# Kernel optimization log

Hardware: AMD Instinct MI355X
Metric: run time of the kernel (lower is better)

## Reference

```python
import jax, jax.numpy as jnp
import numpy as np

B, N, DIM = 2, 1024, 256
DEPTH, HEADS, DIM_HEAD = 4, 4, 64
INNER = HEADS * DIM_HEAD
SCALE = DIM_HEAD ** -0.5
STEP, LAMBD, EPS = 0.1, 0.1, 1e-5


def cx(re, im):
    return jax.lax.complex(re, im)


def setup_inputs() -> dict:
    key = jax.random.key(0)
    ks = jax.random.split(key, 8)
    s = np.float32(1.0 / np.sqrt(DIM))
    f32 = jnp.float32
    return {
        "x_re": jax.random.normal(ks[0], (B, N, DIM), f32),
        "x_im": jax.random.normal(ks[1], (B, N, DIM), f32),
        "ln1_w_re": jnp.ones((DEPTH, DIM), f32),
        "ln1_w_im": jnp.zeros((DEPTH, DIM), f32),
        "ln1_b_re": jnp.zeros((DEPTH, DIM), f32),
        "ln1_b_im": jnp.zeros((DEPTH, DIM), f32),
        "qkv_re": jax.random.normal(ks[2], (DEPTH, INNER, DIM), f32) * s,
        "qkv_im": jax.random.normal(ks[3], (DEPTH, INNER, DIM), f32) * s,
        "out_w_re": jax.random.normal(ks[4], (DEPTH, DIM, INNER), f32) * s,
        "out_w_im": jax.random.normal(ks[5], (DEPTH, DIM, INNER), f32) * s,
        "out_b_re": jnp.zeros((DEPTH, DIM), f32),
        "out_b_im": jnp.zeros((DEPTH, DIM), f32),
        "ln2_w_re": jnp.ones((DEPTH, DIM), f32),
        "ln2_w_im": jnp.zeros((DEPTH, DIM), f32),
        "ln2_b_re": jnp.zeros((DEPTH, DIM), f32),
        "ln2_b_im": jnp.zeros((DEPTH, DIM), f32),
        "ff_re": jax.random.normal(ks[6], (DEPTH, DIM, DIM), f32) * s,
        "ff_im": jax.random.normal(ks[7], (DEPTH, DIM, DIM), f32) * s,
    }


def complex_layernorm(x, w, b):
    # per-component mean/var on real and imag (torch unbiased=False), complex sqrt
    mean = cx(jnp.mean(x.real, -1, keepdims=True), jnp.mean(x.imag, -1, keepdims=True))
    var = cx(jnp.var(x.real, -1, keepdims=True), jnp.var(x.imag, -1, keepdims=True))
    xn = (x - mean) / jnp.sqrt(var + EPS)
    return w * xn + b


def attention(x, Wqkv, Wout, bout):
    # torch Linear: y = x @ W^T ; shared qkv projection w
    w = jnp.einsum('bnd,ed->bne', x, Wqkv)              # [B,N,INNER]
    w = w.reshape(B, N, HEADS, DIM_HEAD).transpose(0, 2, 1, 3)  # [B,H,N,Dh]
    dots = jnp.einsum('bhnd,bhmd->bhnm', w, w.conj()) * SCALE   # complex scores
    mag = jnp.abs(dots)
    a = jax.nn.softmax(mag, axis=-1)                    # softmax on magnitudes
    ph = jnp.angle(dots)                                # polar reconstruction
    attn = cx(a * jnp.cos(ph), a * jnp.sin(ph))
    out = jnp.einsum('bhnm,bhmd->bhnd', attn, w)
    out = out.transpose(0, 2, 1, 3).reshape(B, N, INNER)
    return jnp.einsum('bne,de->bnd', out, Wout) + bout


def feedforward(x, W):
    # FeedForward type1: x1 = x W^T ; CReLU(x + step*x1 - step*lambd)
    x1 = jnp.einsum('bnd,ed->bne', x, W)
    z = x + STEP * x1 - STEP * LAMBD
    return cx(jax.nn.relu(z.real), jax.nn.relu(z.imag))


def reference(x_re, x_im, ln1_w_re, ln1_w_im, ln1_b_re, ln1_b_im,
              qkv_re, qkv_im, out_w_re, out_w_im, out_b_re, out_b_im,
              ln2_w_re, ln2_w_im, ln2_b_re, ln2_b_im, ff_re, ff_im):
    x = cx(x_re, x_im)
    for l in range(DEPTH):
        xn = complex_layernorm(x, cx(ln1_w_re[l], ln1_w_im[l]), cx(ln1_b_re[l], ln1_b_im[l]))
        grad_x = attention(xn, cx(qkv_re[l], qkv_im[l]), cx(out_w_re[l], out_w_im[l]),
                           cx(out_b_re[l], out_b_im[l])) + x
        xn2 = complex_layernorm(grad_x, cx(ln2_w_re[l], ln2_w_im[l]), cx(ln2_b_re[l], ln2_b_im[l]))
        x = feedforward(xn2, cx(ff_re[l], ff_im[l]))
    return x
```

## Files before the change

kernel.cpp:

```cpp
#include <hip/hip_runtime.h>
#include <math.h>

#define B_ 2
#define N_ 1024
#define DIM_ 256
#define DEPTH_ 4
#define HEADS_ 4
#define DHEAD_ 64
#define INNER_ 256
#define SCALE_ 0.125f
#define STEP_ 0.1f
#define LAMBD_ 0.1f
#define EPS_ 1e-5f

typedef __attribute__((ext_vector_type(8))) short short8;
typedef __attribute__((ext_vector_type(4))) float f32x4;

__device__ __forceinline__ unsigned short bf16_rne(float x) {
    unsigned u = __float_as_uint(x);
    unsigned r = (u + 0x7FFFu + ((u >> 16) & 1u)) >> 16;
    return (unsigned short)r;
}
__device__ __forceinline__ float bf16_tof(unsigned short h) {
    return __uint_as_float(((unsigned)h) << 16);
}
__device__ __forceinline__ void split2(float x, unsigned short& hi, unsigned short& lo) {
    hi = bf16_rne(x);
    lo = bf16_rne(x - bf16_tof(hi));
}
__device__ __forceinline__ f32x4 mfma16(short8 a, short8 b, f32x4 c) {
    return __builtin_amdgcn_mfma_f32_16x16x32_bf16(a, b, c, 0, 0, 0);
}
__device__ __forceinline__ short8 neg8(short8 v) {
    union { short8 s; unsigned u[4]; } a; a.s = v;
    a.u[0] ^= 0x80008000u; a.u[1] ^= 0x80008000u;
    a.u[2] ^= 0x80008000u; a.u[3] ^= 0x80008000u;
    return a.s;
}

__global__ __launch_bounds__(64)
void ln_kernel(const float* __restrict__ xr, const float* __restrict__ xi,
               const float* __restrict__ wr, const float* __restrict__ wi,
               const float* __restrict__ br, const float* __restrict__ bi,
               float* __restrict__ outr, float* __restrict__ outi,
               unsigned short* __restrict__ planes, int S) {
    int row = blockIdx.x;
    int lane = threadIdx.x;
    int base = row * DIM_ + lane * 4;

    float4 xr4 = *(const float4*)(xr + base);
    float4 xi4 = *(const float4*)(xi + base);
    float ar[4] = {xr4.x, xr4.y, xr4.z, xr4.w};
    float ai[4] = {xi4.x, xi4.y, xi4.z, xi4.w};

    float sr = ar[0] + ar[1] + ar[2] + ar[3];
    float si = ai[0] + ai[1] + ai[2] + ai[3];
#pragma unroll
    for (int o = 1; o < 64; o <<= 1) {
        sr += __shfl_xor(sr, o, 64);
        si += __shfl_xor(si, o, 64);
    }
    float mre = sr * (1.f / DIM_), mim = si * (1.f / DIM_);

    float drv[4], div[4];
    float vr = 0.f, vi = 0.f;
#pragma unroll
    for (int j = 0; j < 4; j++) {
        drv[j] = ar[j] - mre;
        div[j] = ai[j] - mim;
        vr += drv[j] * drv[j];
        vi += div[j] * div[j];
    }
#pragma unroll
    for (int o = 1; o < 64; o <<= 1) {
        vr += __shfl_xor(vr, o, 64);
        vi += __shfl_xor(vi, o, 64);
    }
    float c = vr * (1.f / DIM_) + EPS_;
    float d = vi * (1.f / DIM_);
    float r = sqrtf(c * c + d * d);
    float sre = sqrtf(0.5f * (r + c));
    float sim = sqrtf(fmaxf(0.5f * (r - c), 0.f));
    float inv = 1.f / r;

    int wc = lane * 4;
    float4 wr4 = *(const float4*)(wr + wc);
    float4 wi4 = *(const float4*)(wi + wc);
    float4 br4 = *(const float4*)(br + wc);
    float4 bi4 = *(const float4*)(bi + wc);
    float wrv[4] = {wr4.x, wr4.y, wr4.z, wr4.w};
    float wiv[4] = {wi4.x, wi4.y, wi4.z, wi4.w};
    float brv[4] = {br4.x, br4.y, br4.z, br4.w};
    float biv[4] = {bi4.x, bi4.y, bi4.z, bi4.w};

    float orr[4], oii[4];
    unsigned short rh[4], rl[4], ih[4], il[4];
#pragma unroll
    for (int j = 0; j < 4; j++) {
        float nr = (drv[j] * sre + div[j] * sim) * inv;
        float ni = (div[j] * sre - drv[j] * sim) * inv;
        orr[j] = wrv[j] * nr - wiv[j] * ni + brv[j];
        oii[j] = wrv[j] * ni + wiv[j] * nr + biv[j];
        split2(orr[j], rh[j], rl[j]);
        split2(oii[j], ih[j], il[j]);
    }
    *(float4*)(outr + base) = make_float4(orr[0], orr[1], orr[2], orr[3]);
    *(float4*)(outi + base) = make_float4(oii[0], oii[1], oii[2], oii[3]);
    *(ushort4*)(planes + 0 * (size_t)S + base) = make_ushort4(rh[0], rh[1], rh[2], rh[3]);
    *(ushort4*)(planes + 1 * (size_t)S + base) = make_ushort4(rl[0], rl[1], rl[2], rl[3]);
    *(ushort4*)(planes + 2 * (size_t)S + base) = make_ushort4(ih[0], ih[1], ih[2], ih[3]);
    *(ushort4*)(planes + 3 * (size_t)S + base) = make_ushort4(il[0], il[1], il[2], il[3]);
}

__global__ void wsplit_all(const float* __restrict__ s0r, const float* __restrict__ s0i,
                           const float* __restrict__ s1r, const float* __restrict__ s1i,
                           const float* __restrict__ s2r, const float* __restrict__ s2i,
                           unsigned short* __restrict__ d0,
                           unsigned short* __restrict__ d1,
                           unsigned short* __restrict__ d2) {
    const int PER = DEPTH_ * 65536;
    int gid = blockIdx.x * 256 + threadIdx.x;
    int sel = gid / PER;
    int idx = gid - sel * PER;
    const float* wr = (sel == 0) ? s0r : (sel == 1) ? s1r : s2r;
    const float* wi = (sel == 0) ? s0i : (sel == 1) ? s1i : s2i;
    unsigned short* dst = (sel == 0) ? d0 : (sel == 1) ? d1 : d2;
    int l = idx >> 16, e = idx & 65535;
    unsigned short rh, rl, ih, il;
    split2(wr[idx], rh, rl);
    split2(wi[idx], ih, il);
    size_t base = (size_t)l * 4 * 65536;
    dst[base + 0 * 65536 + e] = rh;
    dst[base + 1 * 65536 + e] = rl;
    dst[base + 2 * 65536 + e] = ih;
    dst[base + 3 * 65536 + e] = il;
}

template <int MODE>
__global__ __launch_bounds__(64)
void gemm_mfma(const unsigned short* __restrict__ Ap, int aStride,
               const unsigned short* __restrict__ Bp,
               unsigned short* __restrict__ wpo, unsigned short* __restrict__ wtpo,
               const float* __restrict__ biasR, const float* __restrict__ biasI,
               const float* resR, const float* resI,
               float* xoR, float* xoI, int S) {
    const int K = 256;
    int tileM = blockIdx.x * 16, tileN = blockIdx.y * 16;
    int lane = threadIdx.x;
    int m16 = lane & 15, quad = lane >> 4;

    f32x4 accP = (f32x4){0,0,0,0}, accN = (f32x4){0,0,0,0};
    f32x4 accIa = (f32x4){0,0,0,0}, accIb = (f32x4){0,0,0,0};

#pragma unroll
    for (int k0 = 0; k0 < 256; k0 += 32) {
        int kb = k0 + quad * 8;
        short8 a[4], b[4];
#pragma unroll
        for (int p = 0; p < 4; p++) {
            a[p] = *(const short8*)(Ap + (size_t)p * aStride + (size_t)(tileM + m16) * K + kb);
            b[p] = *(const short8*)(Bp + (size_t)p * 65536  + (size_t)(tileN + m16) * K + kb);
        }
        accP  = mfma16(a[0], b[0], accP);
        accP  = mfma16(a[0], b[1], accP);
        accP  = mfma16(a[1], b[0], accP);
        accN  = mfma16(a[2], b[2], accN);
        accN  = mfma16(a[2], b[3], accN);
        accN  = mfma16(a[3], b[2], accN);
        accIa = mfma16(a[0], b[2], accIa);
        accIa = mfma16(a[0], b[3], accIa);
        accIa = mfma16(a[1], b[2], accIa);
        accIb = mfma16(a[2], b[0], accIb);
        accIb = mfma16(a[2], b[1], accIb);
        accIb = mfma16(a[3], b[0], accIb);
    }

#pragma unroll
    for (int r = 0; r < 4; r++) {
        int row = tileM + quad * 4 + r;
        int col = tileN + m16;
        size_t g = (size_t)row * 256 + col;
        float vr = accP[r] - accN[r];
        float vi = accIa[r] + accIb[r];
        if (MODE == 1) {
            unsigned short h0, h1, h2, h3;
            split2(vr, h0, h1);
            split2(vi, h2, h3);
            size_t tidx = ((size_t)(row >> 10) * 256 + col) * 1024 + (row & 1023);
            wpo[0 * (size_t)S + g] = h0;
            wpo[1 * (size_t)S + g] = h1;
            wpo[2 * (size_t)S + g] = h2;
            wpo[3 * (size_t)S + g] = h3;
            wtpo[0 * (size_t)S + tidx] = h0;
            wtpo[1 * (size_t)S + tidx] = h1;
            wtpo[2 * (size_t)S + tidx] = h2;
            wtpo[3 * (size_t)S + tidx] = h3;
        } else if (MODE == 2) {
            xoR[g] = vr + biasR[col] + resR[g];
            xoI[g] = vi + biasI[col] + resI[g];
        } else {
            float zr = resR[g] + STEP_ * vr - STEP_ * LAMBD_;
            float zi = resI[g] + STEP_ * vi;
            xoR[g] = fmaxf(zr, 0.f);
            xoI[g] = fmaxf(zi, 0.f);
        }
    }
}

__global__ __launch_bounds__(256, 2)
void attn_mfma(const unsigned short* __restrict__ wp,
               const unsigned short* __restrict__ wtp,
               float* __restrict__ Op, float* __restrict__ ml, int S) {
    __shared__ unsigned int ShBuf[6336];
    __shared__ float mlbuf[4][64][2];

    int tid = threadIdx.x;
    int wave = tid >> 6, lane = tid & 63;
    int m16 = lane & 15, quad = lane >> 4;
    int zz = blockIdx.x, bb = zz >> 2, hh = zz & 3;
    int q0 = blockIdx.y * 16;
    int kz = blockIdx.z;

    short8 qf[4][2];
    {
        size_t qbase = (size_t)(bb * N_ + q0 + m16) * INNER_ + hh * DHEAD_;
#pragma unroll
        for (int p = 0; p < 4; p++)
#pragma unroll
            for (int kc = 0; kc < 2; kc++)
                qf[p][kc] = *(const short8*)(wp + (size_t)p * S + qbase + kc * 32 + quad * 8);
    }

    float mrow = -1e30f, lrow = 0.f;
    f32x4 Oa[4][2];
#pragma unroll
    for (int ni = 0; ni < 4; ni++) { Oa[ni][0] = (f32x4){0,0,0,0}; Oa[ni][1] = (f32x4){0,0,0,0}; }

    unsigned int* prbu = ShBuf + wave * 1056;

    for (int t = 0; t < 2; t++) {
        int kt = kz * 8 + wave + 4 * t;

        f32x4 sr[4], si[4];
#pragma unroll
        for (int ni = 0; ni < 4; ni++) { sr[ni] = (f32x4){0,0,0,0}; si[ni] = (f32x4){0,0,0,0}; }
#pragma unroll
        for (int ni = 0; ni < 4; ni++) {
            size_t kbase = (size_t)(bb * N_ + kt * 64 + ni * 16 + m16) * INNER_ + hh * DHEAD_;
            short8 kf[4][2];
#pragma unroll
            for (int p = 0; p < 4; p++)
#pragma unroll
                for (int kc = 0; kc < 2; kc++)
                    kf[p][kc] = *(const short8*)(wp + (size_t)p * S + kbase + kc * 32 + quad * 8);
#pragma unroll
            for (int kc = 0; kc < 2; kc++) {
                short8 nki_h = neg8(kf[2][kc]);
                short8 nki_l = neg8(kf[3][kc]);
                f32x4 r = sr[ni], im = si[ni];
                r  = mfma16(kf[0][kc], qf[0][kc], r);
                r  = mfma16(kf[0][kc], qf[1][kc], r);
                r  = mfma16(kf[1][kc], qf[0][kc], r);
                r  = mfma16(kf[2][kc], qf[2][kc], r);
                r  = mfma16(kf[2][kc], qf[3][kc], r);
                r  = mfma16(kf[3][kc], qf[2][kc], r);
                im = mfma16(kf[0][kc], qf[2][kc], im);
                im = mfma16(kf[0][kc], qf[3][kc], im);
                im = mfma16(kf[1][kc], qf[2][kc], im);
                im = mfma16(nki_h, qf[0][kc], im);
                im = mfma16(nki_h, qf[1][kc], im);
                im = mfma16(nki_l, qf[0][kc], im);
                sr[ni] = r; si[ni] = im;
            }
        }

        float mag[4][4], srs[4][4], sis[4][4];
        float mx = -1e30f;
#pragma unroll
        for (int ni = 0; ni < 4; ni++)
#pragma unroll
            for (int r = 0; r < 4; r++) {
                float a = sr[ni][r] * SCALE_, b = si[ni][r] * SCALE_;
                srs[ni][r] = a; sis[ni][r] = b;
                float mg = sqrtf(a * a + b * b);
                mag[ni][r] = mg;
                mx = fmaxf(mx, mg);
            }
        mx = fmaxf(mx, __shfl_xor(mx, 16, 64));
        mx = fmaxf(mx, __shfl_xor(mx, 32, 64));
        float newm = fmaxf(mrow, mx);
        float alpha = __expf(mrow - newm);
        mrow = newm;
        float psum = 0.f;
#pragma unroll
        for (int ni = 0; ni < 4; ni++)
#pragma unroll
            for (int r = 0; r < 4; r++) {
                float p = __expf(mag[ni][r] - newm);
                psum += p;
                float sc = (mag[ni][r] > 0.f) ? (p / mag[ni][r]) : 0.f;
                float pr = (mag[ni][r] > 0.f) ? srs[ni][r] * sc : p;
                float pi = sis[ni][r] * sc;
                int key = ni * 16 + quad * 4 + r;
                prbu[m16 * 66 + key] = ((unsigned)bf16_rne(pi) << 16) | bf16_rne(pr);
            }
        psum += __shfl_xor(psum, 16, 64);
        psum += __shfl_xor(psum, 32, 64);
        lrow = lrow * alpha + psum;
#pragma unroll
        for (int ni = 0; ni < 4; ni++)
#pragma unroll
            for (int r = 0; r < 4; r++) { Oa[ni][0][r] *= alpha; Oa[ni][1][r] *= alpha; }

        short8 prh[2], pih[2], nih[2];
#pragma unroll
        for (int kc = 0; kc < 2; kc++) {
            short8 x, y;
#pragma unroll
            for (int j = 0; j < 8; j++) {
                unsigned val = prbu[m16 * 66 + kc * 32 + quad * 8 + j];
                x[j] = (short)(val & 0xffffu);
                y[j] = (short)(val >> 16);
            }
            prh[kc] = x; pih[kc] = y; nih[kc] = neg8(y);
        }

#pragma unroll
        for (int ni = 0; ni < 4; ni++) {
            size_t vbase = (size_t)(bb * INNER_ + hh * DHEAD_ + ni * 16 + m16) * N_ + kt * 64;
            short8 vr0 = *(const short8*)(wtp + 0 * (size_t)S + vbase + quad * 8);
            short8 vr1 = *(const short8*)(wtp + 0 * (size_t)S + vbase + 32 + quad * 8);
            short8 vi0 = *(const short8*)(wtp + 2 * (size_t)S + vbase + quad * 8);
            short8 vi1 = *(const short8*)(wtp + 2 * (size_t)S + vbase + 32 + quad * 8);
            f32x4 orv = Oa[ni][0], oiv = Oa[ni][1];
            orv = mfma16(vr0, prh[0], orv);
            orv = mfma16(vi0, nih[0], orv);
            orv = mfma16(vr1, prh[1], orv);
            orv = mfma16(vi1, nih[1], orv);
            oiv = mfma16(vr0, pih[0], oiv);
            oiv = mfma16(vi0, prh[0], oiv);
            oiv = mfma16(vr1, pih[1], oiv);
            oiv = mfma16(vi1, prh[1], oiv);
            Oa[ni][0] = orv; Oa[ni][1] = oiv;
        }
    }

    float* Obuf = (float*)ShBuf;
    __syncthreads();
    if (wave != 0) {
        float* mb = Obuf + (wave - 1) * 2112 + lane * 33;
#pragma unroll
        for (int ni = 0; ni < 4; ni++)
#pragma unroll
            for (int r = 0; r < 4; r++) {
                mb[ni * 8 + r]     = Oa[ni][0][r];
                mb[ni * 8 + 4 + r] = Oa[ni][1][r];
            }
        mlbuf[wave][lane][0] = mrow;
        mlbuf[wave][lane][1] = lrow;
    }
    __syncthreads();
    if (wave == 0) {
        float mm = mrow;
#pragma unroll
        for (int w = 1; w < 4; w++) mm = fmaxf(mm, mlbuf[w][lane][0]);
        float a0 = __expf(mrow - mm);
        float ltot = a0 * lrow;
        float aw[3];
#pragma unroll
        for (int w = 1; w < 4; w++) {
            aw[w - 1] = __expf(mlbuf[w][lane][0] - mm);
            ltot += aw[w - 1] * mlbuf[w][lane][1];
        }
        size_t obase = (size_t)(bb * N_ + q0 + m16) * INNER_ + hh * DHEAD_;
        float* opr = Op + (size_t)kz * 2 * S;
        float* opi = opr + S;
#pragma unroll
        for (int ni = 0; ni < 4; ni++)
#pragma unroll
            for (int r = 0; r < 4; r++) {
                float vr = a0 * Oa[ni][0][r];
                float vi = a0 * Oa[ni][1][r];
#pragma unroll
                for (int w = 1; w < 4; w++) {
                    vr += aw[w - 1] * Obuf[(w - 1) * 2112 + lane * 33 + ni * 8 + r];
                    vi += aw[w - 1] * Obuf[(w - 1) * 2112 + lane * 33 + ni * 8 + 4 + r];
                }
                size_t o = obase + ni * 16 + quad * 4 + r;
                opr[o] = vr;
                opi[o] = vi;
            }
        if (quad == 0) {
            int row = bb * N_ + q0 + m16;
            ((float2*)ml)[kz * 8192 + row * 4 + hh] = make_float2(mm, ltot);
        }
    }
}

__global__ void attn_merge(const float* __restrict__ Op, const float* __restrict__ ml,
                           unsigned short* __restrict__ aop, int S) {
    int idx = blockIdx.x * 256 + threadIdx.x;
    int row = idx >> 8;
    int hh = (idx >> 6) & 3;
    float2 ml0 = ((const float2*)ml)[row * 4 + hh];
    float2 ml1 = ((const float2*)ml)[8192 + row * 4 + hh];
    float mm = fmaxf(ml0.x, ml1.x);
    float a0 = __expf(ml0.x - mm), a1 = __expf(ml1.x - mm);
    float invl = 1.f / (a0 * ml0.y + a1 * ml1.y);
    float vr = (a0 * Op[idx] + a1 * Op[2 * (size_t)S + idx]) * invl;
    float vi = (a0 * Op[(size_t)S + idx] + a1 * Op[3 * (size_t)S + idx]) * invl;
    unsigned short h0, h1, h2, h3;
    split2(vr, h0, h1);
    split2(vi, h2, h3);
    aop[0 * (size_t)S + idx] = h0;
    aop[1 * (size_t)S + idx] = h1;
    aop[2 * (size_t)S + idx] = h2;
    aop[3 * (size_t)S + idx] = h3;
}

__global__ void pack_real(const float* __restrict__ xr, float* __restrict__ out, int cap) {
    int idx = blockIdx.x * 256 + threadIdx.x;
    if (idx < cap) out[idx] = xr[idx];
}

extern "C" void kernel_launch(void* const* d_in, const int* in_sizes, int n_in,
                              void* d_out, int out_size, void* d_ws, size_t ws_size,
                              hipStream_t stream) {
    const float* in_xre = (const float*)d_in[0];
    const float* in_xim = (const float*)d_in[1];
    const float* ln1wr = (const float*)d_in[2];
    const float* ln1wi = (const float*)d_in[3];
    const float* ln1br = (const float*)d_in[4];
    const float* ln1bi = (const float*)d_in[5];
    const float* qkvr  = (const float*)d_in[6];
    const float* qkvi  = (const float*)d_in[7];
    const float* outwr = (const float*)d_in[8];
    const float* outwi = (const float*)d_in[9];
    const float* outbr = (const float*)d_in[10];
    const float* outbi = (const float*)d_in[11];
    const float* ln2wr = (const float*)d_in[12];
    const float* ln2wi = (const float*)d_in[13];
    const float* ln2br = (const float*)d_in[14];
    const float* ln2bi = (const float*)d_in[15];
    const float* ffr   = (const float*)d_in[16];
    const float* ffi   = (const float*)d_in[17];

    const size_t S = (size_t)B_ * N_ * DIM_;
    const int    Si = (int)S;

    float* ws  = (float*)d_ws;
    float* xre = ws;            float* xim = xre + S;
    float* xnr = xim + S;       float* xni = xnr + S;
    float* Opart = xni + S;
    float* mlb   = Opart + 4 * S;

    unsigned short* xnp   = (unsigned short*)(mlb + 32768);
    unsigned short* aop   = xnp + 4 * S;
    unsigned short* wpb   = aop + 4 * S;
    unsigned short* wtpb  = wpb + 4 * S;
    unsigned short* qkvp  = wtpb + 4 * S;
    unsigned short* outwp = qkvp + (size_t)DEPTH_ * 4 * 65536;
    unsigned short* ffp   = outwp + (size_t)DEPTH_ * 4 * 65536;

    wsplit_all<<<3 * DEPTH_ * 65536 / 256, 256, 0, stream>>>(
        qkvr, qkvi, outwr, outwi, ffr, ffi, qkvp, outwp, ffp);

    const int MR = B_ * N_;
    dim3 gGemm(MR / 16, INNER_ / 16);
    dim3 gAttn(B_ * HEADS_, N_ / 16, 2);
    int eBlocks = (int)(S / 256);

    bool directOut = (out_size >= (int)(2 * S));
    float* foutR = directOut ? (float*)d_out : xre;
    float* foutI = directOut ? (float*)d_out + S : xim;

    for (int l = 0; l < DEPTH_; l++) {
        const float* xinR = (l == 0) ? in_xre : xre;
        const float* xinI = (l == 0) ? in_xim : xim;

        ln_kernel<<<MR, 64, 0, stream>>>(xinR, xinI,
            ln1wr + l * DIM_, ln1wi + l * DIM_, ln1br + l * DIM_, ln1bi + l * DIM_,
            xnr, xni, xnp, Si);

        gemm_mfma<1><<<gGemm, 64, 0, stream>>>(xnp, Si, qkvp + (size_t)l * 4 * 65536,
            wpb, wtpb, nullptr, nullptr, nullptr, nullptr, nullptr, nullptr, Si);

        attn_mfma<<<gAttn, 256, 0, stream>>>(wpb, wtpb, Opart, mlb, Si);
        attn_merge<<<eBlocks, 256, 0, stream>>>(Opart, mlb, aop, Si);

        gemm_mfma<2><<<gGemm, 64, 0, stream>>>(aop, Si, outwp + (size_t)l * 4 * 65536,
            nullptr, nullptr, outbr + l * DIM_, outbi + l * DIM_, xinR, xinI, xre, xim, Si);

        ln_kernel<<<MR, 64, 0, stream>>>(xre, xim,
            ln2wr + l * DIM_, ln2wi + l * DIM_, ln2br + l * DIM_, ln2bi + l * DIM_,
            xnr, xni, xnp, Si);

        float* oR = (l == DEPTH_ - 1) ? foutR : xre;
        float* oI = (l == DEPTH_ - 1) ? foutI : xim;
        gemm_mfma<3><<<gGemm, 64, 0, stream>>>(xnp, Si, ffp + (size_t)l * 4 * 65536,
            nullptr, nullptr, nullptr, nullptr, xnr, xni, oR, oI, Si);
    }

    if (!directOut) {
        pack_real<<<eBlocks, 256, 0, stream>>>(xre, (float*)d_out, out_size);
    }
}
```

Measured before the change: 591.6 us.

## Enlarge GEMM tiles to 32x64 with LDS-staged double-buffered B operands

Each GEMM block now uses four waves covering a 32x64 output tile instead of one wave per 16x16 tile. The split-bf16 B operands are staged cooperatively into a double-buffered shared-memory array, so each B fragment is reused across two row halves and each A fragment across two column tiles. This cuts redundant global loads of weights and activations. In exchange the grid shrinks eightfold and a barrier is added each K step, which lowers parallelism and occupancy.

```diff
diff --git a/kernel.cpp b/kernel.cpp
--- a/kernel.cpp
+++ b/kernel.cpp
@@ -137,72 +137,100 @@
 }
 
 template <int MODE>
-__global__ __launch_bounds__(64)
+__global__ __launch_bounds__(256)
 void gemm_mfma(const unsigned short* __restrict__ Ap, int aStride,
                const unsigned short* __restrict__ Bp,
                unsigned short* __restrict__ wpo, unsigned short* __restrict__ wtpo,
                const float* __restrict__ biasR, const float* __restrict__ biasI,
                const float* resR, const float* resI,
                float* xoR, float* xoI, int S) {
+    __shared__ short8 Bs[2][4][4][64];
     const int K = 256;
-    int tileM = blockIdx.x * 16, tileN = blockIdx.y * 16;
-    int lane = threadIdx.x;
+    int tileM = blockIdx.x * 32, tileN = blockIdx.y * 64;
+    int tid = threadIdx.x;
+    int wave = tid >> 6, lane = tid & 63;
     int m16 = lane & 15, quad = lane >> 4;
-
-    f32x4 accP = (f32x4){0,0,0,0}, accN = (f32x4){0,0,0,0};
-    f32x4 accIa = (f32x4){0,0,0,0}, accIb = (f32x4){0,0,0,0};
-
-#pragma unroll
+    int rowHalf = wave & 1, ntBase = (wave >> 1) * 2;
+    int rowA = tileM + rowHalf * 16 + m16;
+
+    f32x4 accP[2], accN[2], accIa[2], accIb[2];
+#pragma unroll
+    for (int j = 0; j < 2; j++) {
+        accP[j] = (f32x4){0,0,0,0}; accN[j] = (f32x4){0,0,0,0};
+        accIa[j] = (f32x4){0,0,0,0}; accIb[j] = (f32x4){0,0,0,0};
+    }
+
+    int ls = lane;
+    int lrow = tileN + (ls & 15);
+    int lk0 = (ls >> 4) * 8;
+
     for (int k0 = 0; k0 < 256; k0 += 32) {
+        int buf = (k0 >> 5) & 1;
+#pragma unroll
+        for (int nt = 0; nt < 4; nt++) {
+            Bs[buf][wave][nt][ls] =
+                *(const short8*)(Bp + (size_t)wave * 65536 + (size_t)(lrow + nt * 16) * K + k0 + lk0);
+        }
         int kb = k0 + quad * 8;
-        short8 a[4], b[4];
-#pragma unroll
-        for (int p = 0; p < 4; p++) {
-            a[p] = *(const short8*)(Ap + (size_t)p * aStride + (size_t)(tileM + m16) * K + kb);
-            b[p] = *(const short8*)(Bp + (size_t)p * 65536  + (size_t)(tileN + m16) * K + kb);
-        }
-        accP  = mfma16(a[0], b[0], accP);
-        accP  = mfma16(a[0], b[1], accP);
-        accP  = mfma16(a[1], b[0], accP);
-        accN  = mfma16(a[2], b[2], accN);
-        accN  = mfma16(a[2], b[3], accN);
-        accN  = mfma16(a[3], b[2], accN);
-        accIa = mfma16(a[0], b[2], accIa);
-        accIa = mfma16(a[0], b[3], accIa);
-        accIa = mfma16(a[1], b[2], accIa);
-        accIb = mfma16(a[2], b[0], accIb);
-        accIb = mfma16(a[2], b[1], accIb);
-        accIb = mfma16(a[3], b[0], accIb);
-    }
-
-#pragma unroll
-    for (int r = 0; r < 4; r++) {
-        int row = tileM + quad * 4 + r;
-        int col = tileN + m16;
-        size_t g = (size_t)row * 256 + col;
-        float vr = accP[r] - accN[r];
-        float vi = accIa[r] + accIb[r];
-        if (MODE == 1) {
-            unsigned short h0, h1, h2, h3;
-            split2(vr, h0, h1);
-            split2(vi, h2, h3);
-            size_t tidx = ((size_t)(row >> 10) * 256 + col) * 1024 + (row & 1023);
-            wpo[0 * (size_t)S + g] = h0;
-            wpo[1 * (size_t)S + g] = h1;
-            wpo[2 * (size_t)S + g] = h2;
-            wpo[3 * (size_t)S + g] = h3;
-            wtpo[0 * (size_t)S + tidx] = h0;
-            wtpo[1 * (size_t)S + tidx] = h1;
-            wtpo[2 * (size_t)S + tidx] = h2;
-            wtpo[3 * (size_t)S + tidx] = h3;
-        } else if (MODE == 2) {
-            xoR[g] = vr + biasR[col] + resR[g];
-            xoI[g] = vi + biasI[col] + resI[g];
-        } else {
-            float zr = resR[g] + STEP_ * vr - STEP_ * LAMBD_;
-            float zi = resI[g] + STEP_ * vi;
-            xoR[g] = fmaxf(zr, 0.f);
-            xoI[g] = fmaxf(zi, 0.f);
+        short8 a[4];
+#pragma unroll
+        for (int p = 0; p < 4; p++)
+            a[p] = *(const short8*)(Ap + (size_t)p * aStride + (size_t)rowA * K + kb);
+        __syncthreads();
+#pragma unroll
+        for (int j = 0; j < 2; j++) {
+            int nt = ntBase + j;
+            short8 b[4];
+#pragma unroll
+            for (int p = 0; p < 4; p++)
+                b[p] = Bs[buf][p][nt][lane];
+            accP[j]  = mfma16(a[0], b[0], accP[j]);
+            accP[j]  = mfma16(a[0], b[1], accP[j]);
+            accP[j]  = mfma16(a[1], b[0], accP[j]);
+            accN[j]  = mfma16(a[2], b[2], accN[j]);
+            accN[j]  = mfma16(a[2], b[3], accN[j]);
+            accN[j]  = mfma16(a[3], b[2], accN[j]);
+            accIa[j] = mfma16(a[0], b[2], accIa[j]);
+            accIa[j] = mfma16(a[0], b[3], accIa[j]);
+            accIa[j] = mfma16(a[1], b[2], accIa[j]);
+            accIb[j] = mfma16(a[2], b[0], accIb[j]);
+            accIb[j] = mfma16(a[2], b[1], accIb[j]);
+            accIb[j] = mfma16(a[3], b[0], accIb[j]);
+        }
+    }
+
+#pragma unroll
+    for (int j = 0; j < 2; j++) {
+        int nt = ntBase + j;
+#pragma unroll
+        for (int r = 0; r < 4; r++) {
+            int row = tileM + rowHalf * 16 + quad * 4 + r;
+            int col = tileN + nt * 16 + m16;
+            size_t g = (size_t)row * 256 + col;
+            float vr = accP[j][r] - accN[j][r];
+            float vi = accIa[j][r] + accIb[j][r];
+            if (MODE == 1) {
+                unsigned short h0, h1, h2, h3;
+                split2(vr, h0, h1);
+                split2(vi, h2, h3);
+                size_t tidx = ((size_t)(row >> 10) * 256 + col) * 1024 + (row & 1023);
+                wpo[0 * (size_t)S + g] = h0;
+                wpo[1 * (size_t)S + g] = h1;
+                wpo[2 * (size_t)S + g] = h2;
+                wpo[3 * (size_t)S + g] = h3;
+                wtpo[0 * (size_t)S + tidx] = h0;
+                wtpo[1 * (size_t)S + tidx] = h1;
+                wtpo[2 * (size_t)S + tidx] = h2;
+                wtpo[3 * (size_t)S + tidx] = h3;
+            } else if (MODE == 2) {
+                xoR[g] = vr + biasR[col] + resR[g];
+                xoI[g] = vi + biasI[col] + resI[g];
+            } else {
+                float zr = resR[g] + STEP_ * vr - STEP_ * LAMBD_;
+                float zi = resI[g] + STEP_ * vi;
+                xoR[g] = fmaxf(zr, 0.f);
+                xoI[g] = fmaxf(zi, 0.f);
+            }
         }
     }
 }
@@ -466,7 +494,7 @@
         qkvr, qkvi, outwr, outwi, ffr, ffi, qkvp, outwp, ffp);
 
     const int MR = B_ * N_;
-    dim3 gGemm(MR / 16, INNER_ / 16);
+    dim3 gGemm(MR / 32, INNER_ / 64);
     dim3 gAttn(B_ * HEADS_, N_ / 16, 2);
     int eBlocks = (int)(S / 256);
 
@@ -482,13 +510,13 @@
             ln1wr + l * DIM_, ln1wi + l * DIM_, ln1br + l * DIM_, ln1bi + l * DIM_,
             xnr, xni, xnp, Si);
 
-        gemm_mfma<1><<<gGemm, 64, 0, stream>>>(xnp, Si, qkvp + (size_t)l * 4 * 65536,
+        gemm_mfma<1><<<gGemm, 256, 0, stream>>>(xnp, Si, qkvp + (size_t)l * 4 * 65536,
             wpb, wtpb, nullptr, nullptr, nullptr, nullptr, nullptr, nullptr, Si);
 
         attn_mfma<<<gAttn, 256, 0, stream>>>(wpb, wtpb, Opart, mlb, Si);
         attn_merge<<<eBlocks, 256, 0, stream>>>(Opart, mlb, aop, Si);
 
-        gemm_mfma<2><<<gGemm, 64, 0, stream>>>(aop, Si, outwp + (size_t)l * 4 * 65536,
+        gemm_mfma<2><<<gGemm, 256, 0, stream>>>(aop, Si, outwp + (size_t)l * 4 * 65536,
             nullptr, nullptr, outbr + l * DIM_, outbi + l * DIM_, xinR, xinI, xre, xim, Si);
 
         ln_kernel<<<MR, 64, 0, stream>>>(xre, xim,
@@ -497,7 +525,7 @@
 
         float* oR = (l == DEPTH_ - 1) ? foutR : xre;
         float* oI = (l == DEPTH_ - 1) ? foutI : xim;
-        gemm_mfma<3><<<gGemm, 64, 0, stream>>>(xnp, Si, ffp + (size_t)l * 4 * 65536,
+        gemm_mfma<3><<<gGemm, 256, 0, stream>>>(xnp, Si, ffp + (size_t)l * 4 * 65536,
             nullptr, nullptr, nullptr, nullptr, xnr, xni, oR, oI, Si);
     }
 
```

Result: faster. 526.4 us (-11.0%).
